# Performance work log

Measured on AMD Instinct MI355X. Metric: run time of the kernel, lower is better.

Reference implementation:

```python
import jax, jax.numpy as jnp
import numpy as np

B, S, E, D, L, H = 8, 1024, 512, 1024, 8, 16
HD = D // H                 # 64
ROT = max(HD // 2, 32)      # 32
FF = 4 * D
FUSED = 3 * D + 2 * FF      # q,k,v,ff,ff_gate
EPS = 1e-5


def layer_norm(x, w, b):
    mu = jnp.mean(x, axis=-1, keepdims=True)
    var = jnp.mean(jnp.square(x - mu), axis=-1, keepdims=True)
    return (x - mu) * jax.lax.rsqrt(var + EPS) * w + b


def gelu(x):  # fused_gelu from source (erf form, constant 1.41421)
    return x * 0.5 * (1.0 + jax.scipy.special.erf(x / 1.41421))


def silu(x):
    return x * jax.nn.sigmoid(x)


def rotate_half(x):
    x1, x2 = jnp.split(x, 2, axis=-1)
    return jnp.concatenate([-x2, x1], axis=-1)


def rope_tables(seq_len):
    inv = 1.0 / (10000.0 ** (jnp.arange(0, ROT, 2, dtype=jnp.float32) / ROT))
    freqs = jnp.arange(seq_len, dtype=jnp.float32)[:, None] * inv[None, :]
    emb = jnp.concatenate([freqs, freqs], axis=-1)  # [S, ROT]
    # source caches sin/cos in bfloat16 (precision=torch.bfloat16)
    sin = jnp.sin(emb).astype(jnp.bfloat16).astype(jnp.float32)[None, None]
    cos = jnp.cos(emb).astype(jnp.bfloat16).astype(jnp.float32)[None, None]
    return sin, cos  # [1,1,S,ROT]


def setup_inputs() -> dict:
    key = jax.random.key(0)
    ks = jax.random.split(key, 24)
    std = 0.02
    inp = {
        "noisy_embeds": jax.random.normal(ks[0], (B, S, E), jnp.float32),
        "cond_embeds": jax.random.normal(ks[1], (B, S, E), jnp.float32),
        "prev_embeds": jax.random.normal(ks[2], (B, S, E), jnp.float32),
        "infill_mask": jax.random.uniform(ks[3], (B, S, 1), jnp.float32),
        "attention_mask": jnp.zeros((B, 1, 1, S), jnp.float32),
        "times": jax.random.uniform(ks[4], (B,), jnp.float32),
        # time embedding params
        "fourier_w": jax.random.normal(ks[5], (D // 2, 1), jnp.float32),
        "t1_w": jax.random.normal(ks[6], (D, D), jnp.float32) * std,
        "t1_b": jnp.zeros((D,), jnp.float32),
        "t2_w": jax.random.normal(ks[7], (D, D), jnp.float32) * std,
        "t2_b": jnp.zeros((D,), jnp.float32),
        # input projection
        "in_w": jax.random.normal(ks[8], (D, 4 * E), jnp.float32) * std,
        "in_b": jnp.zeros((D,), jnp.float32),
        # per-layer (stacked) block params
        "ln_w": jnp.ones((L, D), jnp.float32),
        "ln_b": jnp.zeros((L, D), jnp.float32),
        "cond_w": jax.random.normal(ks[9], (L, 2 * D, D), jnp.float32) * std,
        "cond_b": jnp.zeros((L, 2 * D), jnp.float32),
        "proj_w": jax.random.normal(ks[10], (L, FUSED, D), jnp.float32) * std,
        "attn_w": jax.random.normal(ks[11], (L, D, D), jnp.float32) * std,
        "attn_b": jnp.zeros((L, D), jnp.float32),
        "ff_w": jax.random.normal(ks[12], (L, D, FF), jnp.float32) * std,
        "ff_b": jnp.zeros((L, D), jnp.float32),
        # output head
        "outln_w": jnp.ones((D,), jnp.float32),
        "outln_b": jnp.zeros((D,), jnp.float32),
        "out_w": jax.random.normal(ks[13], (E, D), jnp.float32) * std,
        "out_b": jnp.zeros((E,), jnp.float32),
        "fin_w": jnp.ones((E,), jnp.float32),
        "fin_b": jnp.zeros((E,), jnp.float32),
    }
    return inp


def _split_heads(x):  # [B,S,H*hd] -> [B,H,S,hd]
    return x.reshape(B, S, H, HD).transpose(0, 2, 1, 3)


def _forward(noisy_embeds, cond_embeds, prev_embeds, infill_mask, attention_mask,
             times, fourier_w, t1_w, t1_b, t2_w, t2_b, in_w, in_b,
             ln_w, ln_b, cond_w, cond_b, proj_w, attn_w, attn_b, ff_w, ff_b,
             outln_w, outln_b, out_w, out_b, fin_w, fin_b):
    # -- time embedding (Random Fourier + MLP) --
    f = 2.0 * np.pi * (times[:, None] @ fourier_w.T)          # [B, D/2]
    te = jnp.concatenate([jnp.cos(f), jnp.sin(f)], axis=-1)   # [B, D]
    te = gelu(te @ t1_w.T + t1_b) @ t2_w.T + t2_b             # [B, D]
    time_embeds = te[:, None, :]                              # [B, 1, D]

    # -- input projection: cat(noisy, cond, prev, mask broadcast) --
    mask_feat = infill_mask * jnp.ones_like(noisy_embeds)     # [B,S,E]
    x = jnp.concatenate([noisy_embeds, cond_embeds, prev_embeds, mask_feat], axis=-1)
    h = x @ in_w.T + in_b                                     # [B,S,D]

    sin, cos = rope_tables(S)
    sm_scale = HD ** (-0.5)

    for i in range(L):
        units = layer_norm(h, ln_w[i], ln_b[i])
        # FiLM conditioning
        sb = silu(time_embeds) @ cond_w[i].T + cond_b[i]      # [B,1,2D]
        scale, bias = jnp.split(sb, 2, axis=-1)
        units = (1.0 + scale) * units + bias
        # fused projection and split
        proj = units @ proj_w[i].T                            # [B,S,11D]
        q, k, v, ff, ff_gate = jnp.split(
            proj, np.cumsum([D, D, D, FF])[:4].tolist(), axis=-1)
        q, k, v = _split_heads(q), _split_heads(k), _split_heads(v)  # [B,H,S,hd]
        # rotary on first ROT dims
        q = jnp.concatenate(
            [q[..., :ROT] * cos + rotate_half(q[..., :ROT]) * sin, q[..., ROT:]], axis=-1)
        k = jnp.concatenate(
            [k[..., :ROT] * cos + rotate_half(k[..., :ROT]) * sin, k[..., ROT:]], axis=-1)
        # NOTE: source scales BOTH q and k by hd^-0.5 (effective hd^-1)
        score = jnp.einsum('bhsd,bhSd->bhsS', q * sm_scale, k * sm_scale)
        score = score + attention_mask
        w = jax.nn.softmax(score, axis=-1)
        attn = jnp.einsum('bhsS,bhSd->bhsd', w, v)
        merged = attn.transpose(0, 2, 1, 3).reshape(B, S, D)
        attn_out = merged @ attn_w[i].T + attn_b[i]
        ff_out = (ff * gelu(ff_gate)) @ ff_w[i].T + ff_b[i]
        h = h + attn_out + ff_out

    out = layer_norm(h, outln_w, outln_b) @ out_w.T + out_b   # [B,S,E]
    return layer_norm(out, fin_w, fin_b)


def reference(noisy_embeds, cond_embeds, prev_embeds, infill_mask, attention_mask,
              times, fourier_w, t1_w, t1_b, t2_w, t2_b, in_w, in_b,
              ln_w, ln_b, cond_w, cond_b, proj_w, attn_w, attn_b, ff_w, ff_b,
              outln_w, outln_b, out_w, out_b, fin_w, fin_b):
    return _forward(noisy_embeds, cond_embeds, prev_embeds, infill_mask, attention_mask,
                    times, fourier_w, t1_w, t1_b, t2_w, t2_b, in_w, in_b,
                    ln_w, ln_b, cond_w, cond_b, proj_w, attn_w, attn_b, ff_w, ff_b,
                    outln_w, outln_b, out_w, out_b, fin_w, fin_b)
```

## Files before the change

### kernel.cpp

```cpp
#include <hip/hip_runtime.h>
#include <hip/hip_bf16.h>
#include <cstddef>
#include <cstdint>

#define BB 8
#define SS 1024
#define EE 512
#define DD 1024
#define LL 8
#define HH 16
#define HD 64
#define ROT 32
#define FF 4096
#define FUSED 11264
#define NTOK 8192
#define QKVW 3072
#define CATW 5120

using u16 = unsigned short;
typedef __attribute__((ext_vector_type(8))) __bf16 bf16x8;
typedef __attribute__((ext_vector_type(4))) float f32x4;
typedef __attribute__((ext_vector_type(4))) unsigned short u16x4;
typedef __attribute__((ext_vector_type(8))) unsigned short u16x8;

typedef const __attribute__((address_space(1))) void gas_t;
typedef __attribute__((address_space(3))) void las_t;

#define VMCNT8 asm volatile("s_waitcnt vmcnt(8)" ::: "memory")
#define VMCNT0 asm volatile("s_waitcnt vmcnt(0)" ::: "memory")

__device__ __forceinline__ void gld16(const void* g, void* l) {
  __builtin_amdgcn_global_load_lds((gas_t*)g, (las_t*)l, 16, 0, 0);
}

__device__ __forceinline__ float bf2f(u16 u) {
  union { unsigned int i; float f; } v; v.i = ((unsigned int)u) << 16; return v.f;
}
__device__ __forceinline__ u16 f2bf(float f) {
  union { float f; unsigned int i; } v; v.f = f;
  unsigned int u = v.i;
  unsigned int r = u + 0x7FFFu + ((u >> 16) & 1u);
  return (u16)(r >> 16);
}
__device__ __forceinline__ float gelu_f(float x) {
  return x * 0.5f * (1.0f + erff(x / 1.41421f));
}
__device__ __forceinline__ float silu_f(float x) {
  return x / (1.0f + __expf(-x));
}

template <int ACCUM, int OUTBF16>
__global__ __launch_bounds__(256, 2) void gemm_bt(
    const u16* __restrict__ A, const u16* __restrict__ W,
    const float* __restrict__ bias, void* __restrict__ Cp,
    int M, int N, int K) {
  __shared__ __align__(16) u16 As[2][128 * 64];
  __shared__ __align__(16) u16 Bs[2][128 * 64];
  const int tid = threadIdx.x;
  const int w = tid >> 6, lane = tid & 63;
  const int m0 = blockIdx.y * 128, n0 = blockIdx.x * 128;
  const int wm = w >> 1, wn = w & 1;

  f32x4 acc[4][4] = {};

  auto stage = [&](int buf, int k0) {
#pragma unroll
    for (int i = 0; i < 4; i++) {
      const int c = w + i * 4;
      const int r = c * 8 + (lane >> 3);
      const int colb = ((lane & 7) << 4) ^ ((r & 7) << 4);
      gld16(A + (size_t)(m0 + r) * K + k0 + (colb >> 1), &As[buf][c * 512]);
      gld16(W + (size_t)(n0 + r) * K + k0 + (colb >> 1), &Bs[buf][c * 512]);
    }
  };

  const int nt = K >> 6;
  stage(0, 0);

  for (int t = 0; t < nt; t++) {
    const int cur = t & 1;
    if (t + 1 < nt) {
      stage(cur ^ 1, (t + 1) << 6);
      VMCNT8;
    } else {
      VMCNT0;
    }
    __builtin_amdgcn_s_barrier();

    bf16x8 av0[4], bv0[4], av1[4], bv1[4];
#pragma unroll
    for (int m = 0; m < 4; m++) {
      const int row = wm * 64 + m * 16 + (lane & 15);
      const int sw = (row & 7) << 4;
      av0[m] = *(const bf16x8*)((const char*)As[cur] + row * 128 + ((((lane >> 4) << 4)) ^ sw));
      av1[m] = *(const bf16x8*)((const char*)As[cur] + row * 128 + ((64 + ((lane >> 4) << 4)) ^ sw));
    }
#pragma unroll
    for (int n = 0; n < 4; n++) {
      const int row = wn * 64 + n * 16 + (lane & 15);
      const int sw = (row & 7) << 4;
      bv0[n] = *(const bf16x8*)((const char*)Bs[cur] + row * 128 + ((((lane >> 4) << 4)) ^ sw));
      bv1[n] = *(const bf16x8*)((const char*)Bs[cur] + row * 128 + ((64 + ((lane >> 4) << 4)) ^ sw));
    }
    __builtin_amdgcn_s_setprio(1);
#pragma unroll
    for (int m = 0; m < 4; m++)
#pragma unroll
      for (int n = 0; n < 4; n++)
        acc[m][n] = __builtin_amdgcn_mfma_f32_16x16x32_bf16(av0[m], bv0[n], acc[m][n], 0, 0, 0);
#pragma unroll
    for (int m = 0; m < 4; m++)
#pragma unroll
      for (int n = 0; n < 4; n++)
        acc[m][n] = __builtin_amdgcn_mfma_f32_16x16x32_bf16(av1[m], bv1[n], acc[m][n], 0, 0, 0);
    __builtin_amdgcn_s_setprio(0);
    __builtin_amdgcn_s_barrier();
  }

  const int rowb0 = m0 + wm * 64 + ((lane >> 4) << 2);
  const int colb0 = n0 + wn * 64 + (lane & 15);
#pragma unroll
  for (int n = 0; n < 4; n++) {
    const int col = colb0 + n * 16;
    const float bn = bias ? bias[col] : 0.0f;
#pragma unroll
    for (int m = 0; m < 4; m++) {
#pragma unroll
      for (int r = 0; r < 4; r++) {
        const size_t idx = (size_t)(rowb0 + m * 16 + r) * N + col;
        const float v = acc[m][n][r] + bn;
        if (ACCUM) {
          ((float*)Cp)[idx] += v;
        } else if (OUTBF16) {
          ((u16*)Cp)[idx] = f2bf(v);
        } else {
          ((float*)Cp)[idx] = v;
        }
      }
    }
  }
}

template <int GATED>
__global__ __launch_bounds__(512, 2) void gemm_bt256(
    const u16* __restrict__ A, const u16* __restrict__ W,
    void* __restrict__ Cp, int M, int N, int K, int ostride, int ocol0) {
  __shared__ __align__(16) u16 As[2][256 * 64];
  __shared__ __align__(16) u16 Bs[2][256 * 64];
  const int tid = threadIdx.x;
  const int w = tid >> 6, lane = tid & 63;
  const int m0 = blockIdx.y * 256, n0 = blockIdx.x * 256;
  const int wm = w >> 2, wn = w & 3;

  f32x4 acc[8][4] = {};

  auto stage = [&](int buf, int k0) {
#pragma unroll
    for (int i = 0; i < 4; i++) {
      const int c = w + i * 8;
      const int r = c * 8 + (lane >> 3);
      const int colb = ((lane & 7) << 4) ^ ((r & 7) << 4);
      gld16(A + (size_t)(m0 + r) * K + k0 + (colb >> 1), &As[buf][c * 512]);
      gld16(W + (size_t)(n0 + r) * K + k0 + (colb >> 1), &Bs[buf][c * 512]);
    }
  };

  const int nt = K >> 6;
  stage(0, 0);

  for (int t = 0; t < nt; t++) {
    const int cur = t & 1;
    if (t + 1 < nt) {
      stage(cur ^ 1, (t + 1) << 6);
      VMCNT8;
    } else {
      VMCNT0;
    }
    __builtin_amdgcn_s_barrier();

    {
      bf16x8 av0[8], bv0[4];
#pragma unroll
      for (int m = 0; m < 8; m++) {
        const int row = wm * 128 + m * 16 + (lane & 15);
        const int cb = (((lane >> 4) << 4)) ^ ((row & 7) << 4);
        av0[m] = *(const bf16x8*)((const char*)As[cur] + row * 128 + cb);
      }
#pragma unroll
      for (int n = 0; n < 4; n++) {
        const int row = wn * 64 + n * 16 + (lane & 15);
        const int cb = (((lane >> 4) << 4)) ^ ((row & 7) << 4);
        bv0[n] = *(const bf16x8*)((const char*)Bs[cur] + row * 128 + cb);
      }
      __builtin_amdgcn_s_setprio(1);
#pragma unroll
      for (int m = 0; m < 8; m++)
#pragma unroll
        for (int n = 0; n < 4; n++)
          acc[m][n] = __builtin_amdgcn_mfma_f32_16x16x32_bf16(av0[m], bv0[n], acc[m][n], 0, 0, 0);
      __builtin_amdgcn_s_setprio(0);
    }
    {
      bf16x8 av1[8], bv1[4];
#pragma unroll
      for (int m = 0; m < 8; m++) {
        const int row = wm * 128 + m * 16 + (lane & 15);
        const int cb = (64 + ((lane >> 4) << 4)) ^ ((row & 7) << 4);
        av1[m] = *(const bf16x8*)((const char*)As[cur] + row * 128 + cb);
      }
#pragma unroll
      for (int n = 0; n < 4; n++) {
        const int row = wn * 64 + n * 16 + (lane & 15);
        const int cb = (64 + ((lane >> 4) << 4)) ^ ((row & 7) << 4);
        bv1[n] = *(const bf16x8*)((const char*)Bs[cur] + row * 128 + cb);
      }
      __builtin_amdgcn_s_setprio(1);
#pragma unroll
      for (int m = 0; m < 8; m++)
#pragma unroll
        for (int n = 0; n < 4; n++)
          acc[m][n] = __builtin_amdgcn_mfma_f32_16x16x32_bf16(av1[m], bv1[n], acc[m][n], 0, 0, 0);
      __builtin_amdgcn_s_setprio(0);
    }
    __builtin_amdgcn_s_barrier();
  }

  const int rowb0 = m0 + wm * 128 + ((lane >> 4) << 2);
  if (GATED) {
#pragma unroll
    for (int n = 0; n < 4; n += 2) {
      const int outcol = (n0 >> 1) + wn * 32 + ((n >> 1) << 4) + (lane & 15);
#pragma unroll
      for (int m = 0; m < 8; m++)
#pragma unroll
        for (int r = 0; r < 4; r++) {
          const float fv = acc[m][n][r];
          const float gv = acc[m][n + 1][r];
          ((u16*)Cp)[(size_t)(rowb0 + m * 16 + r) * ostride + ocol0 + outcol] =
              f2bf(fv * gelu_f(gv));
        }
    }
  } else {
    const int colb0 = n0 + wn * 64 + (lane & 15);
#pragma unroll
    for (int n = 0; n < 4; n++) {
      const int col = colb0 + n * 16;
#pragma unroll
      for (int m = 0; m < 8; m++)
#pragma unroll
        for (int r = 0; r < 4; r++)
          ((u16*)Cp)[(size_t)(rowb0 + m * 16 + r) * N + col] = f2bf(acc[m][n][r]);
    }
  }
}

__global__ __launch_bounds__(256, 2) void attn_fwd(
    const u16* __restrict__ qr, const u16* __restrict__ kr,
    const u16* __restrict__ vt, const float* __restrict__ mask,
    u16* __restrict__ acat) {
  __shared__ __align__(16) u16 Ks[2][128 * 64];
  __shared__ __align__(16) u16 Vs[2][64 * 128];
  __shared__ __align__(16) u16 Ps[4][16 * 128];
  const int tid = threadIdx.x, w = tid >> 6, lane = tid & 63;
  const int g = blockIdx.x;
  const int j = g >> 3;
  const int bh = (g & 7) + ((j >> 4) << 3);
  const int qx = j & 15;
  const int b = bh >> 4;
  const int q0 = qx * 64 + w * 16;
  const u16* Qb = qr + (size_t)bh * SS * HD;
  const u16* Kb = kr + (size_t)bh * SS * HD;
  const u16* Vb = vt + (size_t)bh * HD * SS;
  const float* mb = mask + (size_t)b * SS;

  bf16x8 qf0, qf1;
  {
    const int qrow = q0 + (lane & 15);
    const u16* qp = Qb + (size_t)qrow * HD + ((lane >> 4) << 3);
    qf0 = *(const bf16x8*)qp;
    qf1 = *(const bf16x8*)(qp + 32);
  }

  float mrun[4], srun[4];
  f32x4 acc[4] = {};
#pragma unroll
  for (int r = 0; r < 4; r++) { mrun[r] = -1e30f; srun[r] = 0.0f; }

  u16* pw = &Ps[w][0];

  auto stage = [&](int buf, int kv0) {
#pragma unroll
    for (int i = 0; i < 4; i++) {
      const int c = w + i * 4;
      {
        const int r = c * 8 + (lane >> 3);
        const int colb = ((lane & 7) << 4) ^ ((r & 7) << 4);
        gld16(Kb + (size_t)(kv0 + r) * HD + (colb >> 1), &Ks[buf][c * 512]);
      }
      {
        const int d = c * 4 + (lane >> 4);
        const int colb = ((lane & 15) << 4) ^ ((d & 7) << 4);
        gld16(Vb + (size_t)d * SS + kv0 + (colb >> 1), &Vs[buf][c * 512]);
      }
    }
  };

  stage(0, 0);
  __syncthreads();

  for (int t = 0; t < 8; t++) {
    const int cur = t & 1;
    const int kv0 = t * 128;
    if (t < 7) stage(cur ^ 1, kv0 + 128);

    f32x4 p[8];
    __builtin_amdgcn_s_setprio(1);
#pragma unroll
    for (int blk = 0; blk < 8; blk++) {
      const int row = blk * 16 + (lane & 15);
      const int swz = (row & 7) << 4;
      const bf16x8 k0v = *(const bf16x8*)((const char*)Ks[cur] + row * 128 + ((((lane >> 4) << 4)) ^ swz));
      const bf16x8 k1v = *(const bf16x8*)((const char*)Ks[cur] + row * 128 + ((64 + ((lane >> 4) << 4)) ^ swz));
      f32x4 z = {};
      p[blk] = __builtin_amdgcn_mfma_f32_16x16x32_bf16(qf0, k0v, z, 0, 0, 0);
      p[blk] = __builtin_amdgcn_mfma_f32_16x16x32_bf16(qf1, k1v, p[blk], 0, 0, 0);
    }
    __builtin_amdgcn_s_setprio(0);

    float mv[8];
#pragma unroll
    for (int blk = 0; blk < 8; blk++) mv[blk] = mb[kv0 + blk * 16 + (lane & 15)];
#pragma unroll
    for (int blk = 0; blk < 8; blk++)
#pragma unroll
      for (int r = 0; r < 4; r++) p[blk][r] = p[blk][r] * (1.0f / 64.0f) + mv[blk];

    float fac[4];
#pragma unroll
    for (int r = 0; r < 4; r++) {
      float tm = p[0][r];
#pragma unroll
      for (int blk = 1; blk < 8; blk++) tm = fmaxf(tm, p[blk][r]);
      tm = fmaxf(tm, __shfl_xor(tm, 1));
      tm = fmaxf(tm, __shfl_xor(tm, 2));
      tm = fmaxf(tm, __shfl_xor(tm, 4));
      tm = fmaxf(tm, __shfl_xor(tm, 8));
      const float mn = fmaxf(mrun[r], tm);
      fac[r] = __expf(mrun[r] - mn);
      mrun[r] = mn;
      float rs = 0.0f;
#pragma unroll
      for (int blk = 0; blk < 8; blk++) {
        const float e = __expf(p[blk][r] - mn);
        p[blk][r] = e;
        rs += e;
      }
      rs += __shfl_xor(rs, 1);
      rs += __shfl_xor(rs, 2);
      rs += __shfl_xor(rs, 4);
      rs += __shfl_xor(rs, 8);
      srun[r] = srun[r] * fac[r] + rs;
    }
#pragma unroll
    for (int dblk = 0; dblk < 4; dblk++)
#pragma unroll
      for (int r = 0; r < 4; r++) acc[dblk][r] *= fac[r];

#pragma unroll
    for (int blk = 0; blk < 8; blk++)
#pragma unroll
      for (int r = 0; r < 4; r++) {
        const int q = ((lane >> 4) << 2) + r;
        pw[(q * 128 + blk * 16 + (lane & 15)) ^ ((q & 7) << 3)] = f2bf(p[blk][r]);
      }

    bf16x8 pa[4];
#pragma unroll
    for (int ks = 0; ks < 4; ks++) {
      const int q = lane & 15;
      pa[ks] = *(const bf16x8*)(pw + ((q * 128 + ks * 32 + ((lane >> 4) << 3)) ^ ((q & 7) << 3)));
    }

    __builtin_amdgcn_s_setprio(1);
#pragma unroll
    for (int dblk = 0; dblk < 4; dblk++) {
      const int drow = dblk * 16 + (lane & 15);
      const int swz = (drow & 7) << 4;
#pragma unroll
      for (int ks = 0; ks < 4; ks++) {
        const bf16x8 vv = *(const bf16x8*)((const char*)Vs[cur] + drow * 256 + ((ks * 64 + ((lane >> 4) << 4)) ^ swz));
        acc[dblk] = __builtin_amdgcn_mfma_f32_16x16x32_bf16(pa[ks], vv, acc[dblk], 0, 0, 0);
      }
    }
    __builtin_amdgcn_s_setprio(0);

    __syncthreads();
  }

#pragma unroll
  for (int dblk = 0; dblk < 4; dblk++)
#pragma unroll
    for (int r = 0; r < 4; r++) {
      const int sq = q0 + ((lane >> 4) << 2) + r;
      const int d = dblk * 16 + (lane & 15);
      acat[((size_t)b * SS + sq) * CATW + (bh & 15) * HD + d] = f2bf(acc[dblk][r] / srun[r]);
    }
}

__global__ __launch_bounds__(256) void ln_mod(
    const float* __restrict__ x, const float* __restrict__ lw,
    const float* __restrict__ lb, const float* __restrict__ sb,
    u16* __restrict__ out) {
  const int row = blockIdx.x, tid = threadIdx.x;
  const float4 v = ((const float4*)(x + (size_t)row * DD))[tid];
  float vv[4] = {v.x, v.y, v.z, v.w};
  float s = vv[0] + vv[1] + vv[2] + vv[3];
  float q = vv[0] * vv[0] + vv[1] * vv[1] + vv[2] * vv[2] + vv[3] * vv[3];
  for (int off = 1; off < 64; off <<= 1) {
    s += __shfl_xor(s, off);
    q += __shfl_xor(q, off);
  }
  __shared__ float red[8];
  const int w = tid >> 6, lane = tid & 63;
  if (lane == 0) { red[w] = s; red[4 + w] = q; }
  __syncthreads();
  s = red[0] + red[1] + red[2] + red[3];
  q = red[4] + red[5] + red[6] + red[7];
  const float mu = s * (1.0f / DD);
  const float inv = rsqrtf(q * (1.0f / DD) - mu * mu + 1e-5f);
  const int b = row >> 10;
  u16x4 o;
#pragma unroll
  for (int j = 0; j < 4; j++) {
    const int d = tid * 4 + j;
    float g = (vv[j] - mu) * inv * lw[d] + lb[d];
    if (sb) g = (1.0f + sb[(size_t)b * 2048 + d]) * g + sb[(size_t)b * 2048 + DD + d];
    o[j] = f2bf(g);
  }
  *(u16x4*)(out + (size_t)row * DD + tid * 4) = o;
}

__global__ __launch_bounds__(128) void ln_fin(
    const float* __restrict__ x, const float* __restrict__ w_,
    const float* __restrict__ b_, float* __restrict__ out) {
  const int row = blockIdx.x, tid = threadIdx.x;
  const float4 v = ((const float4*)(x + (size_t)row * EE))[tid];
  float vv[4] = {v.x, v.y, v.z, v.w};
  float s = vv[0] + vv[1] + vv[2] + vv[3];
  float q = vv[0] * vv[0] + vv[1] * vv[1] + vv[2] * vv[2] + vv[3] * vv[3];
  for (int off = 1; off < 64; off <<= 1) {
    s += __shfl_xor(s, off);
    q += __shfl_xor(q, off);
  }
  __shared__ float red[4];
  const int w = tid >> 6, lane = tid & 63;
  if (lane == 0) { red[w] = s; red[2 + w] = q; }
  __syncthreads();
  s = red[0] + red[1];
  q = red[2] + red[3];
  const float mu = s * (1.0f / EE);
  const float inv = rsqrtf(q * (1.0f / EE) - mu * mu + 1e-5f);
  float4 o;
  o.x = (vv[0] - mu) * inv * w_[tid * 4 + 0] + b_[tid * 4 + 0];
  o.y = (vv[1] - mu) * inv * w_[tid * 4 + 1] + b_[tid * 4 + 1];
  o.z = (vv[2] - mu) * inv * w_[tid * 4 + 2] + b_[tid * 4 + 2];
  o.w = (vv[3] - mu) * inv * w_[tid * 4 + 3] + b_[tid * 4 + 3];
  ((float4*)(out + (size_t)row * EE))[tid] = o;
}

template <int IA, int OA>
__global__ __launch_bounds__(256) void vec_gemm(
    const float* __restrict__ in, const float* __restrict__ W,
    const float* __restrict__ bias, float* __restrict__ out, int N, int K) {
  const int n = blockIdx.x * 256 + threadIdx.x;
  const int b = blockIdx.y, l = blockIdx.z;
  const float* ir = in + (size_t)b * K;
  const float* wr = W + ((size_t)l * N + n) * K;
  float s = bias[(size_t)l * N + n];
  for (int k = 0; k < K; k += 4) {
    float4 a = *(const float4*)(ir + k);
    const float4 ww = *(const float4*)(wr + k);
    if (IA) { a.x = silu_f(a.x); a.y = silu_f(a.y); a.z = silu_f(a.z); a.w = silu_f(a.w); }
    s += a.x * ww.x + a.y * ww.y + a.z * ww.z + a.w * ww.w;
  }
  if (OA) s = gelu_f(s);
  out[((size_t)l * gridDim.y + b) * N + n] = s;
}

__global__ void time_fourier(const float* __restrict__ times,
                             const float* __restrict__ fw, float* __restrict__ te0) {
  const int j = blockIdx.x * 256 + threadIdx.x;
  const int b = blockIdx.y;
  const float f = 6.28318530717958647692f * times[b] * fw[j];
  te0[(size_t)b * DD + j] = cosf(f);
  te0[(size_t)b * DD + 512 + j] = sinf(f);
}

__global__ void rope_tab(float* __restrict__ st, float* __restrict__ ct) {
  const int s = blockIdx.x;
  const int j = threadIdx.x;
  const int i = j & 15;
  const float inv = powf(10000.0f, -(float)i * (1.0f / 16.0f));
  const float f = (float)s * inv;
  st[s * 32 + j] = bf2f(f2bf(sinf(f)));
  ct[s * 32 + j] = bf2f(f2bf(cosf(f)));
}

__global__ void build_x(const float* __restrict__ a, const float* __restrict__ b,
                        const float* __restrict__ c, const float* __restrict__ m,
                        u16* __restrict__ x) {
  const size_t i4 = ((size_t)blockIdx.x * 256 + threadIdx.x) * 4;
  if (i4 >= (size_t)NTOK * 2048) return;
  const size_t tok = i4 >> 11;
  const int e = (int)(i4 & 2047);
  float4 v;
  if (e < 512)       v = *(const float4*)(a + tok * 512 + e);
  else if (e < 1024) v = *(const float4*)(b + tok * 512 + (e - 512));
  else if (e < 1536) v = *(const float4*)(c + tok * 512 + (e - 1024));
  else { const float mm = m[tok]; v = make_float4(mm, mm, mm, mm); }
  u16x4 o;
  o[0] = f2bf(v.x); o[1] = f2bf(v.y); o[2] = f2bf(v.z); o[3] = f2bf(v.w);
  *(u16x4*)(x + i4) = o;
}

__global__ void rope_qk(const u16* __restrict__ proj, const float* __restrict__ st,
                        const float* __restrict__ ct, u16* __restrict__ q,
                        u16* __restrict__ k) {
  const size_t idx = (size_t)blockIdx.x * 256 + threadIdx.x;
  const size_t tok = idx >> 10;
  const int hd = (int)(idx & 1023);
  const int hh = hd >> 6, d = hd & 63;
  const int s = (int)(tok & 1023);
  const size_t bb = tok >> 10;
  const u16* pr = proj + tok * QKVW;
  float qv = bf2f(pr[hd]);
  float kv = bf2f(pr[DD + hd]);
  if (d < ROT) {
    const float cs = ct[s * 32 + d], sn = st[s * 32 + d];
    const int pidx = hd - d + ((d < 16) ? d + 16 : d - 16);
    const float qp = bf2f(pr[pidx]);
    const float kp = bf2f(pr[DD + pidx]);
    const float sg = (d < 16) ? -1.0f : 1.0f;
    qv = qv * cs + sg * qp * sn;
    kv = kv * cs + sg * kp * sn;
  }
  const size_t o = ((bb * HH + hh) * SS + s) * HD + d;
  q[o] = f2bf(qv);
  k[o] = f2bf(kv);
}

__global__ __launch_bounds__(256) void transp_v(const u16* __restrict__ proj,
                                                u16* __restrict__ v) {
  __shared__ u16 tile[64 * 72];
  const int tid = threadIdx.x;
  const int s0 = blockIdx.x * 64, h = blockIdx.y, b = blockIdx.z;
  {
    const int sl = tid >> 2, qd = (tid & 3) * 16;
    const u16* src = proj + (size_t)(b * SS + s0 + sl) * QKVW + 2 * DD + h * 64 + qd;
    const u16x8 a0 = *(const u16x8*)src;
    const u16x8 a1 = *(const u16x8*)(src + 8);
    *(u16x8*)&tile[sl * 72 + qd] = a0;
    *(u16x8*)&tile[sl * 72 + qd + 8] = a1;
  }
  __syncthreads();
  {
    const int dl = tid >> 2, qs = (tid & 3) * 16;
    u16x8 o0, o1;
#pragma unroll
    for (int j = 0; j < 8; j++) o0[j] = tile[(qs + j) * 72 + dl];
#pragma unroll
    for (int j = 0; j < 8; j++) o1[j] = tile[(qs + 8 + j) * 72 + dl];
    u16* dst = v + ((size_t)(b * HH + h) * HD + dl) * SS + s0 + qs;
    *(u16x8*)dst = o0;
    *(u16x8*)(dst + 8) = o1;
  }
}

__global__ void cast_bf16(const float* __restrict__ in, u16* __restrict__ out, size_t n4) {
  const size_t i = (size_t)blockIdx.x * 256 + threadIdx.x;
  if (i >= n4) return;
  const float4 v = ((const float4*)in)[i];
  u16x4 o;
  o[0] = f2bf(v.x); o[1] = f2bf(v.y); o[2] = f2bf(v.z); o[3] = f2bf(v.w);
  ((u16x4*)out)[i] = o;
}

__global__ void cast_q(const float* __restrict__ src, u16* __restrict__ dst) {
  const int i = blockIdx.x * 256 + threadIdx.x;
  const int l = blockIdx.y;
  const int r = i >> 7, cb = (i & 127) * 8;
  const float* s = src + ((size_t)l * FUSED + r) * DD + cb;
  const float4 a = *(const float4*)s;
  const float4 b = *(const float4*)(s + 4);
  u16x8 o;
  o[0] = f2bf(a.x); o[1] = f2bf(a.y); o[2] = f2bf(a.z); o[3] = f2bf(a.w);
  o[4] = f2bf(b.x); o[5] = f2bf(b.y); o[6] = f2bf(b.z); o[7] = f2bf(b.w);
  *(u16x8*)(dst + ((size_t)l * QKVW + r) * DD + cb) = o;
}

__global__ void cast_ffg(const float* __restrict__ src, u16* __restrict__ dst) {
  const int i = blockIdx.x * 256 + threadIdx.x;
  const int l = blockIdx.y;
  const int r = i >> 7, cb = (i & 127) * 8;
  const int t16 = r >> 4, pos = r & 15;
  const int j = (t16 >> 1) * 16 + pos;
  const int srow = (t16 & 1) ? (3 * DD + FF + j) : (3 * DD + j);
  const float* s = src + ((size_t)l * FUSED + srow) * DD + cb;
  const float4 a = *(const float4*)s;
  const float4 b = *(const float4*)(s + 4);
  u16x8 o;
  o[0] = f2bf(a.x); o[1] = f2bf(a.y); o[2] = f2bf(a.z); o[3] = f2bf(a.w);
  o[4] = f2bf(b.x); o[5] = f2bf(b.y); o[6] = f2bf(b.z); o[7] = f2bf(b.w);
  *(u16x8*)(dst + ((size_t)l * 8192 + r) * DD + cb) = o;
}

__global__ void cast_catw(const float* __restrict__ aw, const float* __restrict__ fw,
                          u16* __restrict__ dst) {
  const int i = blockIdx.x * 256 + threadIdx.x;
  const int l = blockIdx.y;
  const int n = i / 640, cb = (i % 640) * 8;
  const float* s = (cb < DD) ? (aw + ((size_t)l * DD + n) * DD + cb)
                             : (fw + ((size_t)l * DD + n) * FF + (cb - DD));
  const float4 a = *(const float4*)s;
  const float4 b = *(const float4*)(s + 4);
  u16x8 o;
  o[0] = f2bf(a.x); o[1] = f2bf(a.y); o[2] = f2bf(a.z); o[3] = f2bf(a.w);
  o[4] = f2bf(b.x); o[5] = f2bf(b.y); o[6] = f2bf(b.z); o[7] = f2bf(b.w);
  *(u16x8*)(dst + ((size_t)l * DD + n) * CATW + cb) = o;
}

__global__ void add_bias(const float* __restrict__ a, const float* __restrict__ b,
                         float* __restrict__ o, int n) {
  const int i = blockIdx.x * 256 + threadIdx.x;
  if (i < n) o[i] = a[i] + b[i];
}

extern "C" void kernel_launch(void* const* d_in, const int* in_sizes, int n_in,
                              void* d_out, int out_size, void* d_ws, size_t ws_size,
                              hipStream_t stream) {
  const float* noisy   = (const float*)d_in[0];
  const float* condi   = (const float*)d_in[1];
  const float* prev    = (const float*)d_in[2];
  const float* infill  = (const float*)d_in[3];
  const float* amask   = (const float*)d_in[4];
  const float* times   = (const float*)d_in[5];
  const float* fourier = (const float*)d_in[6];
  const float* t1_w    = (const float*)d_in[7];
  const float* t1_b    = (const float*)d_in[8];
  const float* t2_w    = (const float*)d_in[9];
  const float* t2_b    = (const float*)d_in[10];
  const float* in_w    = (const float*)d_in[11];
  const float* in_b    = (const float*)d_in[12];
  const float* ln_w    = (const float*)d_in[13];
  const float* ln_b    = (const float*)d_in[14];
  const float* cond_w  = (const float*)d_in[15];
  const float* cond_b  = (const float*)d_in[16];
  const float* proj_w  = (const float*)d_in[17];
  const float* attn_w  = (const float*)d_in[18];
  const float* attn_b  = (const float*)d_in[19];
  const float* ff_w    = (const float*)d_in[20];
  const float* ff_b    = (const float*)d_in[21];
  const float* outln_w = (const float*)d_in[22];
  const float* outln_b = (const float*)d_in[23];
  const float* out_w   = (const float*)d_in[24];
  const float* out_b   = (const float*)d_in[25];
  const float* fin_w   = (const float*)d_in[26];
  const float* fin_b   = (const float*)d_in[27];
  float* outp = (float*)d_out;

  char* p = (char*)d_ws;
  auto alloc = [&](size_t bytes) -> char* {
    char* r = p;
    p += (bytes + 255) & ~(size_t)255;
    return r;
  };
  u16* in_w_h    = (u16*)alloc((size_t)DD * 2048 * 2);
  u16* projq_w_h = (u16*)alloc((size_t)LL * QKVW * DD * 2);
  u16* ffg_w_h   = (u16*)alloc((size_t)LL * 8192 * DD * 2);
  u16* cat_w_h   = (u16*)alloc((size_t)LL * DD * CATW * 2);
  float* cat_b   = (float*)alloc((size_t)LL * DD * 4);
  u16* out_w_h   = (u16*)alloc((size_t)EE * DD * 2);
  float* te0 = (float*)alloc((size_t)BB * DD * 4);
  float* te1 = (float*)alloc((size_t)BB * DD * 4);
  float* te2 = (float*)alloc((size_t)BB * DD * 4);
  float* sb  = (float*)alloc((size_t)LL * BB * 2048 * 4);
  float* stab = (float*)alloc((size_t)SS * 32 * 4);
  float* ctab = (float*)alloc((size_t)SS * 32 * 4);
  u16* xb    = (u16*)alloc((size_t)NTOK * 2048 * 2);
  float* h   = (float*)alloc((size_t)NTOK * DD * 4);
  u16* units = (u16*)alloc((size_t)NTOK * DD * 2);
  u16* projq = (u16*)alloc((size_t)NTOK * QKVW * 2);
  u16* qrb   = (u16*)alloc((size_t)NTOK * DD * 2);
  u16* krb   = (u16*)alloc((size_t)NTOK * DD * 2);
  u16* vtb   = (u16*)alloc((size_t)NTOK * DD * 2);
  u16* acat  = (u16*)alloc((size_t)NTOK * CATW * 2);
  u16* hn    = (u16*)alloc((size_t)NTOK * DD * 2);
  float* ob  = (float*)alloc((size_t)NTOK * EE * 4);

  auto castN = [&](const float* src, u16* dst, size_t n) {
    const size_t n4 = n / 4;
    cast_bf16<<<dim3((unsigned)((n4 + 255) / 256)), dim3(256), 0, stream>>>(src, dst, n4);
  };
  castN(in_w, in_w_h, (size_t)DD * 2048);
  cast_q<<<dim3(QKVW * 128 / 256, LL), 256, 0, stream>>>(proj_w, projq_w_h);
  cast_ffg<<<dim3(8192 * 128 / 256, LL), 256, 0, stream>>>(proj_w, ffg_w_h);
  cast_catw<<<dim3(DD * 640 / 256, LL), 256, 0, stream>>>(attn_w, ff_w, cat_w_h);
  add_bias<<<dim3(LL * DD / 256), 256, 0, stream>>>(attn_b, ff_b, cat_b, LL * DD);
  castN(out_w, out_w_h, (size_t)EE * DD);

  time_fourier<<<dim3(2, BB), 256, 0, stream>>>(times, fourier, te0);
  vec_gemm<0, 1><<<dim3(4, BB, 1), 256, 0, stream>>>(te0, t1_w, t1_b, te1, 1024, 1024);
  vec_gemm<0, 0><<<dim3(4, BB, 1), 256, 0, stream>>>(te1, t2_w, t2_b, te2, 1024, 1024);
  vec_gemm<1, 0><<<dim3(8, BB, LL), 256, 0, stream>>>(te2, cond_w, cond_b, sb, 2048, 1024);
  rope_tab<<<SS, 32, 0, stream>>>(stab, ctab);
  build_x<<<16384, 256, 0, stream>>>(noisy, condi, prev, infill, xb);
  gemm_bt<0, 0><<<dim3(DD / 128, NTOK / 128), 256, 0, stream>>>(xb, in_w_h, in_b, h, NTOK, DD, 2048);

  for (int l = 0; l < LL; l++) {
    ln_mod<<<NTOK, 256, 0, stream>>>(h, ln_w + (size_t)l * DD, ln_b + (size_t)l * DD,
                                     sb + (size_t)l * BB * 2048, units);
    gemm_bt<0, 1><<<dim3(QKVW / 128, NTOK / 128), 256, 0, stream>>>(
        units, projq_w_h + (size_t)l * QKVW * DD, nullptr, projq, NTOK, QKVW, DD);
    gemm_bt256<1><<<dim3(8192 / 256, NTOK / 256), 512, 0, stream>>>(
        units, ffg_w_h + (size_t)l * 8192 * DD, acat, NTOK, 8192, DD, CATW, DD);
    rope_qk<<<32768, 256, 0, stream>>>(projq, stab, ctab, qrb, krb);
    transp_v<<<dim3(SS / 64, HH, BB), 256, 0, stream>>>(projq, vtb);
    attn_fwd<<<dim3(2048), 256, 0, stream>>>(qrb, krb, vtb, amask, acat);
    gemm_bt<1, 0><<<dim3(DD / 128, NTOK / 128), 256, 0, stream>>>(
        acat, cat_w_h + (size_t)l * DD * CATW, cat_b + (size_t)l * DD, h, NTOK, DD, CATW);
  }

  ln_mod<<<NTOK, 256, 0, stream>>>(h, outln_w, outln_b, nullptr, hn);
  gemm_bt<0, 0><<<dim3(EE / 128, NTOK / 128), 256, 0, stream>>>(hn, out_w_h, out_b, ob, NTOK, EE, DD);
  ln_fin<<<NTOK, 128, 0, stream>>>(ob, fin_w, fin_b, outp);
}
```

Baseline: 4.804 ms.

## Fuse RoPE with V transpose and transpose QK^T in flash attention softmax

The separate rope_qk and transp_v kernels are merged into one rope_all kernel that applies RoPE to q and k with 16-element vector loads and stores, and transposes V in the same pass. This saves a launch and reads the projection buffer once with wider accesses. In attention, the MFMA operands are swapped so each lane holds one query row's scores, so the row max and sum need only two cross-lane shuffles, and the mask is read as float4. The rescale of the accumulator is skipped when no running max grows, at the cost of extra shuffles to redistribute the scale factors.

```diff
diff --git a/kernel.cpp b/kernel.cpp
--- a/kernel.cpp
+++ b/kernel.cpp
@@ -272,19 +272,18 @@
   const u16* Kb = kr + (size_t)bh * SS * HD;
   const u16* Vb = vt + (size_t)bh * HD * SS;
   const float* mb = mask + (size_t)b * SS;
+  const int lq = lane & 15, lg = lane >> 4;
 
   bf16x8 qf0, qf1;
   {
-    const int qrow = q0 + (lane & 15);
-    const u16* qp = Qb + (size_t)qrow * HD + ((lane >> 4) << 3);
+    const int qrow = q0 + lq;
+    const u16* qp = Qb + (size_t)qrow * HD + (lg << 3);
     qf0 = *(const bf16x8*)qp;
     qf1 = *(const bf16x8*)(qp + 32);
   }
 
-  float mrun[4], srun[4];
+  float mrun = -1e30f, srun = 0.0f;
   f32x4 acc[4] = {};
-#pragma unroll
-  for (int r = 0; r < 4; r++) { mrun[r] = -1e30f; srun[r] = 0.0f; }
 
   u16* pw = &Ps[w][0];
 
@@ -298,8 +297,8 @@
         gld16(Kb + (size_t)(kv0 + r) * HD + (colb >> 1), &Ks[buf][c * 512]);
       }
       {
-        const int d = c * 4 + (lane >> 4);
-        const int colb = ((lane & 15) << 4) ^ ((d & 7) << 4);
+        const int d = c * 4 + lg;
+        const int colb = (lq << 4) ^ ((d & 7) << 4);
         gld16(Vb + (size_t)d * SS + kv0 + (colb >> 1), &Vs[buf][c * 512]);
       }
     }
@@ -317,93 +316,93 @@
     __builtin_amdgcn_s_setprio(1);
 #pragma unroll
     for (int blk = 0; blk < 8; blk++) {
-      const int row = blk * 16 + (lane & 15);
+      const int row = blk * 16 + lq;
       const int swz = (row & 7) << 4;
-      const bf16x8 k0v = *(const bf16x8*)((const char*)Ks[cur] + row * 128 + ((((lane >> 4) << 4)) ^ swz));
-      const bf16x8 k1v = *(const bf16x8*)((const char*)Ks[cur] + row * 128 + ((64 + ((lane >> 4) << 4)) ^ swz));
+      const bf16x8 k0v = *(const bf16x8*)((const char*)Ks[cur] + row * 128 + (((lg << 4)) ^ swz));
+      const bf16x8 k1v = *(const bf16x8*)((const char*)Ks[cur] + row * 128 + ((64 + (lg << 4)) ^ swz));
       f32x4 z = {};
-      p[blk] = __builtin_amdgcn_mfma_f32_16x16x32_bf16(qf0, k0v, z, 0, 0, 0);
-      p[blk] = __builtin_amdgcn_mfma_f32_16x16x32_bf16(qf1, k1v, p[blk], 0, 0, 0);
+      p[blk] = __builtin_amdgcn_mfma_f32_16x16x32_bf16(k0v, qf0, z, 0, 0, 0);
+      p[blk] = __builtin_amdgcn_mfma_f32_16x16x32_bf16(k1v, qf1, p[blk], 0, 0, 0);
     }
     __builtin_amdgcn_s_setprio(0);
 
-    float mv[8];
-#pragma unroll
-    for (int blk = 0; blk < 8; blk++) mv[blk] = mb[kv0 + blk * 16 + (lane & 15)];
+#pragma unroll
+    for (int blk = 0; blk < 8; blk++) {
+      const float4 m4 = *(const float4*)(mb + kv0 + blk * 16 + (lg << 2));
+      p[blk][0] = p[blk][0] * (1.0f / 64.0f) + m4.x;
+      p[blk][1] = p[blk][1] * (1.0f / 64.0f) + m4.y;
+      p[blk][2] = p[blk][2] * (1.0f / 64.0f) + m4.z;
+      p[blk][3] = p[blk][3] * (1.0f / 64.0f) + m4.w;
+    }
+
+    float mrow = p[0][0];
 #pragma unroll
     for (int blk = 0; blk < 8; blk++)
 #pragma unroll
-      for (int r = 0; r < 4; r++) p[blk][r] = p[blk][r] * (1.0f / 64.0f) + mv[blk];
-
-    float fac[4];
+      for (int r = 0; r < 4; r++) mrow = fmaxf(mrow, p[blk][r]);
+    mrow = fmaxf(mrow, __shfl_xor(mrow, 16));
+    mrow = fmaxf(mrow, __shfl_xor(mrow, 32));
+
+    if (__any(mrow > mrun)) {
+      const float mn = fmaxf(mrun, mrow);
+      const float facq = __expf(mrun - mn);
+      mrun = mn;
+      srun *= facq;
+      float fac[4];
+#pragma unroll
+      for (int r = 0; r < 4; r++)
+        fac[r] = __shfl(facq, (lane & 48) | ((lg << 2) + r));
+#pragma unroll
+      for (int dblk = 0; dblk < 4; dblk++)
+#pragma unroll
+        for (int r = 0; r < 4; r++) acc[dblk][r] *= fac[r];
+    }
+
+    float rs = 0.0f;
+#pragma unroll
+    for (int blk = 0; blk < 8; blk++)
+#pragma unroll
+      for (int r = 0; r < 4; r++) {
+        const float e = __expf(p[blk][r] - mrun);
+        rs += e;
+        pw[((lq * 128) + blk * 16 + (lg << 2) + r) ^ ((lq & 7) << 3)] = f2bf(e);
+      }
+    rs += __shfl_xor(rs, 16);
+    rs += __shfl_xor(rs, 32);
+    srun += rs;
+
+    bf16x8 pa[4];
+#pragma unroll
+    for (int ks = 0; ks < 4; ks++)
+      pa[ks] = *(const bf16x8*)(pw + ((lq * 128 + ks * 32 + (lg << 3)) ^ ((lq & 7) << 3)));
+
+    __builtin_amdgcn_s_setprio(1);
+#pragma unroll
+    for (int dblk = 0; dblk < 4; dblk++) {
+      const int drow = dblk * 16 + lq;
+      const int swz = (drow & 7) << 4;
+#pragma unroll
+      for (int ks = 0; ks < 4; ks++) {
+        const bf16x8 vv = *(const bf16x8*)((const char*)Vs[cur] + drow * 256 + ((ks * 64 + (lg << 4)) ^ swz));
+        acc[dblk] = __builtin_amdgcn_mfma_f32_16x16x32_bf16(pa[ks], vv, acc[dblk], 0, 0, 0);
+      }
+    }
+    __builtin_amdgcn_s_setprio(0);
+
+    __syncthreads();
+  }
+
+  float sden[4];
+#pragma unroll
+  for (int r = 0; r < 4; r++)
+    sden[r] = __shfl(srun, (lane & 48) | ((lg << 2) + r));
+#pragma unroll
+  for (int dblk = 0; dblk < 4; dblk++)
 #pragma unroll
     for (int r = 0; r < 4; r++) {
-      float tm = p[0][r];
-#pragma unroll
-      for (int blk = 1; blk < 8; blk++) tm = fmaxf(tm, p[blk][r]);
-      tm = fmaxf(tm, __shfl_xor(tm, 1));
-      tm = fmaxf(tm, __shfl_xor(tm, 2));
-      tm = fmaxf(tm, __shfl_xor(tm, 4));
-      tm = fmaxf(tm, __shfl_xor(tm, 8));
-      const float mn = fmaxf(mrun[r], tm);
-      fac[r] = __expf(mrun[r] - mn);
-      mrun[r] = mn;
-      float rs = 0.0f;
-#pragma unroll
-      for (int blk = 0; blk < 8; blk++) {
-        const float e = __expf(p[blk][r] - mn);
-        p[blk][r] = e;
-        rs += e;
-      }
-      rs += __shfl_xor(rs, 1);
-      rs += __shfl_xor(rs, 2);
-      rs += __shfl_xor(rs, 4);
-      rs += __shfl_xor(rs, 8);
-      srun[r] = srun[r] * fac[r] + rs;
-    }
-#pragma unroll
-    for (int dblk = 0; dblk < 4; dblk++)
-#pragma unroll
-      for (int r = 0; r < 4; r++) acc[dblk][r] *= fac[r];
-
-#pragma unroll
-    for (int blk = 0; blk < 8; blk++)
-#pragma unroll
-      for (int r = 0; r < 4; r++) {
-        const int q = ((lane >> 4) << 2) + r;
-        pw[(q * 128 + blk * 16 + (lane & 15)) ^ ((q & 7) << 3)] = f2bf(p[blk][r]);
-      }
-
-    bf16x8 pa[4];
-#pragma unroll
-    for (int ks = 0; ks < 4; ks++) {
-      const int q = lane & 15;
-      pa[ks] = *(const bf16x8*)(pw + ((q * 128 + ks * 32 + ((lane >> 4) << 3)) ^ ((q & 7) << 3)));
-    }
-
-    __builtin_amdgcn_s_setprio(1);
-#pragma unroll
-    for (int dblk = 0; dblk < 4; dblk++) {
-      const int drow = dblk * 16 + (lane & 15);
-      const int swz = (drow & 7) << 4;
-#pragma unroll
-      for (int ks = 0; ks < 4; ks++) {
-        const bf16x8 vv = *(const bf16x8*)((const char*)Vs[cur] + drow * 256 + ((ks * 64 + ((lane >> 4) << 4)) ^ swz));
-        acc[dblk] = __builtin_amdgcn_mfma_f32_16x16x32_bf16(pa[ks], vv, acc[dblk], 0, 0, 0);
-      }
-    }
-    __builtin_amdgcn_s_setprio(0);
-
-    __syncthreads();
-  }
-
-#pragma unroll
-  for (int dblk = 0; dblk < 4; dblk++)
-#pragma unroll
-    for (int r = 0; r < 4; r++) {
-      const int sq = q0 + ((lane >> 4) << 2) + r;
-      const int d = dblk * 16 + (lane & 15);
-      acat[((size_t)b * SS + sq) * CATW + (bh & 15) * HD + d] = f2bf(acc[dblk][r] / srun[r]);
+      const int sq = q0 + (lg << 2) + r;
+      const int d = dblk * 16 + lq;
+      acat[((size_t)b * SS + sq) * CATW + (bh & 15) * HD + d] = f2bf(acc[dblk][r] / sden[r]);
     }
 }
 
@@ -523,46 +522,60 @@
   *(u16x4*)(x + i4) = o;
 }
 
-__global__ void rope_qk(const u16* __restrict__ proj, const float* __restrict__ st,
-                        const float* __restrict__ ct, u16* __restrict__ q,
-                        u16* __restrict__ k) {
-  const size_t idx = (size_t)blockIdx.x * 256 + threadIdx.x;
-  const size_t tok = idx >> 10;
-  const int hd = (int)(idx & 1023);
-  const int hh = hd >> 6, d = hd & 63;
-  const int s = (int)(tok & 1023);
-  const size_t bb = tok >> 10;
-  const u16* pr = proj + tok * QKVW;
-  float qv = bf2f(pr[hd]);
-  float kv = bf2f(pr[DD + hd]);
-  if (d < ROT) {
-    const float cs = ct[s * 32 + d], sn = st[s * 32 + d];
-    const int pidx = hd - d + ((d < 16) ? d + 16 : d - 16);
-    const float qp = bf2f(pr[pidx]);
-    const float kp = bf2f(pr[DD + pidx]);
-    const float sg = (d < 16) ? -1.0f : 1.0f;
-    qv = qv * cs + sg * qp * sn;
-    kv = kv * cs + sg * kp * sn;
-  }
-  const size_t o = ((bb * HH + hh) * SS + s) * HD + d;
-  q[o] = f2bf(qv);
-  k[o] = f2bf(kv);
-}
-
-__global__ __launch_bounds__(256) void transp_v(const u16* __restrict__ proj,
-                                                u16* __restrict__ v) {
+__global__ __launch_bounds__(256) void rope_all(
+    const u16* __restrict__ proj, const float* __restrict__ st,
+    const float* __restrict__ ct, u16* __restrict__ q, u16* __restrict__ k,
+    u16* __restrict__ v) {
   __shared__ u16 tile[64 * 72];
   const int tid = threadIdx.x;
   const int s0 = blockIdx.x * 64, h = blockIdx.y, b = blockIdx.z;
+  const int sl = tid >> 2, c = tid & 3;
+  const int s = s0 + sl;
+  const u16* pr = proj + (size_t)(b * SS + s) * QKVW + h * 64;
+
   {
-    const int sl = tid >> 2, qd = (tid & 3) * 16;
-    const u16* src = proj + (size_t)(b * SS + s0 + sl) * QKVW + 2 * DD + h * 64 + qd;
-    const u16x8 a0 = *(const u16x8*)src;
-    const u16x8 a1 = *(const u16x8*)(src + 8);
-    *(u16x8*)&tile[sl * 72 + qd] = a0;
-    *(u16x8*)&tile[sl * 72 + qd + 8] = a1;
-  }
+    const u16x8 a0 = *(const u16x8*)(pr + 2 * DD + c * 16);
+    const u16x8 a1 = *(const u16x8*)(pr + 2 * DD + c * 16 + 8);
+    *(u16x8*)&tile[sl * 72 + c * 16] = a0;
+    *(u16x8*)&tile[sl * 72 + c * 16 + 8] = a1;
+  }
+
+  {
+    const int d0 = c * 16;
+    u16 qv[16], kv[16], qo[16], ko[16];
+    *(u16x8*)&qv[0] = *(const u16x8*)(pr + d0);
+    *(u16x8*)&qv[8] = *(const u16x8*)(pr + d0 + 8);
+    *(u16x8*)&kv[0] = *(const u16x8*)(pr + DD + d0);
+    *(u16x8*)&kv[8] = *(const u16x8*)(pr + DD + d0 + 8);
+    if (c < 2) {
+      const int dp = (c ^ 1) * 16;
+      u16 qp[16], kp[16];
+      *(u16x8*)&qp[0] = *(const u16x8*)(pr + dp);
+      *(u16x8*)&qp[8] = *(const u16x8*)(pr + dp + 8);
+      *(u16x8*)&kp[0] = *(const u16x8*)(pr + DD + dp);
+      *(u16x8*)&kp[8] = *(const u16x8*)(pr + DD + dp + 8);
+      const float sg = (c == 0) ? -1.0f : 1.0f;
+#pragma unroll
+      for (int j = 0; j < 16; j++) {
+        const int d = d0 + j;
+        const float cs = ct[s * 32 + d], sn = st[s * 32 + d];
+        qo[j] = f2bf(bf2f(qv[j]) * cs + sg * bf2f(qp[j]) * sn);
+        ko[j] = f2bf(bf2f(kv[j]) * cs + sg * bf2f(kp[j]) * sn);
+      }
+    } else {
+#pragma unroll
+      for (int j = 0; j < 16; j++) { qo[j] = qv[j]; ko[j] = kv[j]; }
+    }
+    u16* qd = q + ((size_t)(b * HH + h) * SS + s) * HD + d0;
+    u16* kd = k + ((size_t)(b * HH + h) * SS + s) * HD + d0;
+    *(u16x8*)qd = *(u16x8*)&qo[0];
+    *(u16x8*)(qd + 8) = *(u16x8*)&qo[8];
+    *(u16x8*)kd = *(u16x8*)&ko[0];
+    *(u16x8*)(kd + 8) = *(u16x8*)&ko[8];
+  }
+
   __syncthreads();
+
   {
     const int dl = tid >> 2, qs = (tid & 3) * 16;
     u16x8 o0, o1;
@@ -723,8 +736,7 @@
         units, projq_w_h + (size_t)l * QKVW * DD, nullptr, projq, NTOK, QKVW, DD);
     gemm_bt256<1><<<dim3(8192 / 256, NTOK / 256), 512, 0, stream>>>(
         units, ffg_w_h + (size_t)l * 8192 * DD, acat, NTOK, 8192, DD, CATW, DD);
-    rope_qk<<<32768, 256, 0, stream>>>(projq, stab, ctab, qrb, krb);
-    transp_v<<<dim3(SS / 64, HH, BB), 256, 0, stream>>>(projq, vtb);
+    rope_all<<<dim3(SS / 64, HH, BB), 256, 0, stream>>>(projq, stab, ctab, qrb, krb, vtb);
     attn_fwd<<<dim3(2048), 256, 0, stream>>>(qrb, krb, vtb, amask, acat);
     gemm_bt<1, 0><<<dim3(DD / 128, NTOK / 128), 256, 0, stream>>>(
         acat, cat_w_h + (size_t)l * DD * CATW, cat_b + (size_t)l * DD, h, NTOK, DD, CATW);
```

Result: faster. 4.702 ms (-2.1%).
